# Optimization experiments

Hardware: AMD Instinct MI355X
Metric: run time of the kernel (lower is better)

Reference implementation:

```python
import jax, jax.numpy as jnp
import numpy as np

B = 262144
NODE_ROWS, EDGE_ROWS, D = 19, 36, 4
KEEP = 4


def _make_sparse(key, rows):
    # each sample has exactly KEEP nonzero rows at random (sorted) positions
    k1, k2 = jax.random.split(key)
    perm = jnp.argsort(jax.random.uniform(k1, (B, rows)), axis=1)
    idx = jnp.sort(perm[:, :KEEP], axis=1)                      # (B, KEEP)
    vals = jax.random.normal(k2, (B, KEEP, D), dtype=jnp.float32) + 0.1
    x = jnp.zeros((B, rows, D), dtype=jnp.float32)
    x = x.at[jnp.arange(B)[:, None], idx].set(vals)
    return x.reshape(B, rows * D)


def setup_inputs() -> dict:
    key = jax.random.key(0)
    kn, ke, k1, k2, k3 = jax.random.split(key, 5)
    node = _make_sparse(kn, NODE_ROWS)   # (B, 76)
    edge = _make_sparse(ke, EDGE_ROWS)   # (B, 144)
    # MLP params (torch Linear default-ish init, stored as (in, out))
    def lin(k, fin, fout):
        ka, kb = jax.random.split(k)
        s = 1.0 / np.sqrt(fin)
        W = jax.random.uniform(ka, (fin, fout), jnp.float32, -s, s)
        b = jax.random.uniform(kb, (fout,), jnp.float32, -s, s)
        return W, b
    W1, b1 = lin(k1, 32, 256)
    W2, b2 = lin(k2, 256, 128)
    W3, b3 = lin(k3, 128, 34)
    return {"node": node, "edge": edge, "W1": W1, "b1": b1,
            "W2": W2, "b2": b2, "W3": W3, "b3": b3}


def _compact4(x):
    # x: (B, R, D) -> first 4 nonzero rows per sample, order preserved: (B, 4, D)
    mask = jnp.any(x != 0, axis=-1)                              # (B, R)
    idx = jnp.argsort(~mask, axis=1, stable=True)[:, :KEEP]      # (B, 4)
    return jnp.take_along_axis(x, idx[:, :, None], axis=1)


def reference(node, edge, W1, b1, W2, b2, W3, b3):
    n = _compact4(node.reshape(-1, NODE_ROWS, D))                # (B, 4, 4)
    e = _compact4(edge.reshape(-1, EDGE_ROWS, D))                # (B, 4, 4)
    x = jnp.concatenate([n, e], axis=-2).reshape(-1, 8 * D)      # (B, 32)
    x = jax.nn.relu(x @ W1 + b1)
    x = jax.nn.relu(x @ W2 + b2)
    x = x @ W3 + b3                                              # (B, 34)
    return jax.nn.log_softmax(x, axis=1)
```

## Files before the change

kernel.cpp:

```cpp
#include <hip/hip_runtime.h>
#include <stdint.h>
#include <stddef.h>

typedef __bf16 bf16;
typedef __attribute__((ext_vector_type(8))) __bf16 bf16x8;
typedef __attribute__((ext_vector_type(4))) __bf16 bf16x4;
typedef __attribute__((ext_vector_type(4))) float  f32x4;
typedef __attribute__((ext_vector_type(16))) float f32x16;

#define W1OFF  0
#define W2OFF  (16*1024)
#define W3OFF  (80*1024)
#define BIOFF  (96*1024)
#define BI2OFF (BIOFF + 1024)
#define BI3OFF (BIOFF + 1536)
#define IMGSZ  (96*1024 + 1792)
#define NCHUNK (IMGSZ/16)
#define PERW   4096
#define LDSSZ  (IMGSZ + 8*PERW)

#define SWZ(s) ((((s)>>1)&3)<<4)

#define MFMA32(a,b,c) __builtin_amdgcn_mfma_f32_32x32x16_bf16((a),(b),(c),0,0,0)

__global__ void prep_kernel(const float* __restrict__ W1, const float* __restrict__ b1,
                            const float* __restrict__ W2, const float* __restrict__ b2,
                            const float* __restrict__ W3, const float* __restrict__ b3,
                            char* __restrict__ img)
{
  int tid = blockIdx.x * 256 + threadIdx.x;
  if (tid < 1024) {
    int frag = tid >> 6, l = tid & 63;
    int c = frag >> 1, t = frag & 1, hi = l >> 5;
    int n = c * 32 + (l & 31), k0 = t * 16 + 8 * hi;
    bf16x8 v;
    #pragma unroll
    for (int j = 0; j < 8; ++j) v[j] = (bf16)W1[(size_t)(k0 + j) * 256 + n];
    *(bf16x8*)(img + (size_t)tid * 16) = v;
  } else if (tid < 5120) {
    int e = tid - 1024, frag = e >> 6, l = e & 63;
    int nt2 = frag >> 4, c = (frag >> 1) & 7, t = frag & 1, hi = l >> 5;
    int n = nt2 * 32 + (l & 31), k0 = c * 32 + t * 16 + 8 * hi;
    bf16x8 v;
    #pragma unroll
    for (int j = 0; j < 8; ++j) v[j] = (bf16)W2[(size_t)(k0 + j) * 128 + n];
    *(bf16x8*)(img + W2OFF + (size_t)e * 16) = v;
  } else if (tid < 6144) {
    int e = tid - 5120, frag = e >> 6, l = e & 63;
    int nt3 = frag >> 3, c2 = (frag >> 1) & 3, t = frag & 1, hi = l >> 5;
    int n = nt3 * 32 + (l & 31), k0 = c2 * 32 + t * 16 + 8 * hi;
    bf16x8 v;
    #pragma unroll
    for (int j = 0; j < 8; ++j)
      v[j] = (n < 34) ? (bf16)W3[(size_t)(k0 + j) * 34 + n] : (bf16)0.f;
    *(bf16x8*)(img + W3OFF + (size_t)e * 16) = v;
  } else if (tid < 6144 + 448) {
    int e = tid - 6144;
    int le, chunk, idx; const float* bsrc; char* dst; int nb;
    if (e < 256)      { le = e;       bsrc = b1; dst = img + BIOFF;  nb = 34; chunk = le >> 5; }
    else if (e < 384) { le = e - 256; bsrc = b2; dst = img + BI2OFF; nb = 1000; chunk = le >> 5; }
    else              { le = e - 384; bsrc = b3; dst = img + BI3OFF; nb = 34; chunk = le >> 5; }
    idx = le & 31;
    int hi = idx >> 4, reg = idx & 15;
    int f = chunk * 32 + (reg & 3) + 8 * (reg >> 2) + 4 * hi;
    float v;
    if (e < 256)      v = b1[f];
    else if (e < 384) v = b2[f];
    else              v = (f < 34) ? b3[f] : 0.f;
    (void)bsrc; (void)nb;
    ((float*)dst)[le] = v;
  }
}

__global__ __launch_bounds__(512, 2) void mlp_kernel(
    const float* __restrict__ node, const float* __restrict__ edge,
    const char* __restrict__ img, float* __restrict__ out)
{
  __shared__ __align__(16) char sm[LDSSZ];
  const int tid  = threadIdx.x;
  const int lane = tid & 63;
  const int w    = tid >> 6;
  const int blk  = blockIdx.x;

  for (int c = tid; c < NCHUNK; c += 512)
    *(f32x4*)(sm + (size_t)c * 16) = *(const f32x4*)(img + (size_t)c * 16);
  __syncthreads();

  char* const xw  = sm + IMGSZ + w * PERW;
  char* const stg = xw + 2048;

  const int col = lane & 31;
  const int hi  = lane >> 5;
  const int swz = (col >> 1) & 3;
  const int cl  = lane & 3;
  const int sl  = lane >> 2;

  const float4* const np = (const float4*)node;
  const float4* const ep = (const float4*)edge;

  float4 nf[5], ef[9];

  auto issue_loads = [&](int sbase) {
    const int s = sbase + sl;
    #pragma unroll
    for (int i = 0; i < 5; ++i) {
      const int r = cl + 4 * i;
      nf[i] = (r < 19) ? np[(size_t)s * 19 + r] : make_float4(0.f, 0.f, 0.f, 0.f);
    }
    #pragma unroll
    for (int i = 0; i < 9; ++i)
      ef[i] = ep[(size_t)s * 36 + cl + 4 * i];
  };

  auto compact = [&](char* dst) {
    uint32_t nm = 0; unsigned long long em = 0;
    #pragma unroll
    for (int i = 0; i < 5; ++i) {
      const int r = cl + 4 * i;
      if (r < 19 && (nf[i].x != 0.f || nf[i].y != 0.f || nf[i].z != 0.f || nf[i].w != 0.f))
        nm |= (1u << r);
    }
    #pragma unroll
    for (int i = 0; i < 9; ++i) {
      const int r = cl + 4 * i;
      if (ef[i].x != 0.f || ef[i].y != 0.f || ef[i].z != 0.f || ef[i].w != 0.f)
        em |= (1ull << r);
    }
    nm |= __shfl_xor(nm, 1); nm |= __shfl_xor(nm, 2);
    em |= __shfl_xor(em, 1); em |= __shfl_xor(em, 2);
    bf16x4 zb; zb[0] = (bf16)0.f; zb[1] = (bf16)0.f; zb[2] = (bf16)0.f; zb[3] = (bf16)0.f;
    *(bf16x4*)(dst + sl * 64 + ((8 * cl)      ^ SWZ(sl))) = zb;
    *(bf16x4*)(dst + sl * 64 + ((8 * cl + 32) ^ SWZ(sl))) = zb;
    #pragma unroll
    for (int i = 0; i < 5; ++i) {
      const int r = cl + 4 * i;
      if (r < 19 && ((nm >> r) & 1u)) {
        const int slot = __popc(nm & ((1u << r) - 1u));
        if (slot < 4) {
          bf16x4 pk; pk[0] = (bf16)nf[i].x; pk[1] = (bf16)nf[i].y; pk[2] = (bf16)nf[i].z; pk[3] = (bf16)nf[i].w;
          *(bf16x4*)(dst + sl * 64 + ((8 * slot) ^ SWZ(sl))) = pk;
        }
      }
    }
    #pragma unroll
    for (int i = 0; i < 9; ++i) {
      const int r = cl + 4 * i;
      if ((em >> r) & 1ull) {
        const int slot = __popcll(em & ((1ull << r) - 1ull));
        if (slot < 4) {
          bf16x4 pk; pk[0] = (bf16)ef[i].x; pk[1] = (bf16)ef[i].y; pk[2] = (bf16)ef[i].z; pk[3] = (bf16)ef[i].w;
          *(bf16x4*)(dst + sl * 64 + ((32 + 8 * slot) ^ SWZ(sl))) = pk;
        }
      }
    }
  };

  auto ldbias = [&](const char* p) -> f32x16 {
    const f32x4* q4 = (const f32x4*)(p + hi * 64);
    f32x4 q0 = q4[0], q1 = q4[1], q2 = q4[2], q3 = q4[3];
    f32x16 r;
    #pragma unroll
    for (int i = 0; i < 4; ++i) { r[i] = q0[i]; r[4+i] = q1[i]; r[8+i] = q2[i]; r[12+i] = q3[i]; }
    return r;
  };

  #pragma unroll 1
  for (int p = 0; p < 4; ++p) {
    const int S = blk * 1024 + p * 256 + w * 32;

    issue_loads(S);       compact(xw);
    issue_loads(S + 16);  compact(xw + 1024);

    bf16x8 xf0 = *(const bf16x8*)(xw + col * 64 + ((hi * 16)      ^ SWZ(col)));
    bf16x8 xf1 = *(const bf16x8*)(xw + col * 64 + ((32 + hi * 16) ^ SWZ(col)));

    f32x16 acc2[4];
    #pragma unroll
    for (int nt2 = 0; nt2 < 4; ++nt2) acc2[nt2] = ldbias(sm + BI2OFF + nt2 * 128);

    #pragma unroll 1
    for (int c = 0; c < 8; ++c) {
      __builtin_amdgcn_sched_barrier(0);
      f32x16 d = ldbias(sm + BIOFF + c * 128);
      bf16x8 w10 = *(const bf16x8*)(sm + W1OFF + (c * 2 + 0) * 1024 + lane * 16);
      bf16x8 w11 = *(const bf16x8*)(sm + W1OFF + (c * 2 + 1) * 1024 + lane * 16);
      d = MFMA32(w10, xf0, d);
      d = MFMA32(w11, xf1, d);
      #pragma unroll
      for (int q = 0; q < 4; ++q) {
        bf16x4 pk;
        #pragma unroll
        for (int i = 0; i < 4; ++i) pk[i] = (bf16)fmaxf(d[4 * q + i], 0.f);
        *(bf16x4*)(stg + col * 64 + (((q ^ swz) << 4) + hi * 8)) = pk;
      }
      bf16x8 sf0 = *(const bf16x8*)(stg + col * 64 + (((0 + hi) ^ swz) << 4));
      bf16x8 sf1 = *(const bf16x8*)(stg + col * 64 + (((2 + hi) ^ swz) << 4));
      #pragma unroll
      for (int nt2 = 0; nt2 < 4; ++nt2) {
        bf16x8 a0 = *(const bf16x8*)(sm + W2OFF + ((nt2 * 8 + c) * 2 + 0) * 1024 + lane * 16);
        bf16x8 a1 = *(const bf16x8*)(sm + W2OFF + ((nt2 * 8 + c) * 2 + 1) * 1024 + lane * 16);
        acc2[nt2] = MFMA32(a0, sf0, acc2[nt2]);
        acc2[nt2] = MFMA32(a1, sf1, acc2[nt2]);
      }
    }

    f32x16 acc3[2];
    acc3[0] = ldbias(sm + BI3OFF + 0);
    acc3[1] = ldbias(sm + BI3OFF + 128);

    #pragma unroll
    for (int c2 = 0; c2 < 4; ++c2) {
      #pragma unroll
      for (int q = 0; q < 4; ++q) {
        bf16x4 pk;
        #pragma unroll
        for (int i = 0; i < 4; ++i) pk[i] = (bf16)fmaxf(acc2[c2][4 * q + i], 0.f);
        *(bf16x4*)(stg + col * 64 + (((q ^ swz) << 4) + hi * 8)) = pk;
      }
      bf16x8 sf0 = *(const bf16x8*)(stg + col * 64 + (((0 + hi) ^ swz) << 4));
      bf16x8 sf1 = *(const bf16x8*)(stg + col * 64 + (((2 + hi) ^ swz) << 4));
      #pragma unroll
      for (int nt3 = 0; nt3 < 2; ++nt3) {
        bf16x8 a0 = *(const bf16x8*)(sm + W3OFF + ((nt3 * 4 + c2) * 2 + 0) * 1024 + lane * 16);
        bf16x8 a1 = *(const bf16x8*)(sm + W3OFF + ((nt3 * 4 + c2) * 2 + 1) * 1024 + lane * 16);
        acc3[nt3] = MFMA32(a0, sf0, acc3[nt3]);
        acc3[nt3] = MFMA32(a1, sf1, acc3[nt3]);
      }
    }

    float mx = acc3[0][0];
    #pragma unroll
    for (int i = 1; i < 16; ++i) mx = fmaxf(mx, acc3[0][i]);
    if (hi == 0) { mx = fmaxf(mx, acc3[1][0]); mx = fmaxf(mx, acc3[1][1]); }
    mx = fmaxf(mx, __shfl_xor(mx, 32));
    float sum = 0.f;
    #pragma unroll
    for (int i = 0; i < 16; ++i) sum += __expf(acc3[0][i] - mx);
    if (hi == 0) sum += __expf(acc3[1][0] - mx) + __expf(acc3[1][1] - mx);
    sum += __shfl_xor(sum, 32);
    const float lse = mx + __logf(sum);

    float* orow = out + (size_t)(S + col) * 34;
    #pragma unroll
    for (int q = 0; q < 4; ++q) {
      *(float2*)(orow + 8 * q + 4 * hi)     = make_float2(acc3[0][4 * q]     - lse, acc3[0][4 * q + 1] - lse);
      *(float2*)(orow + 8 * q + 4 * hi + 2) = make_float2(acc3[0][4 * q + 2] - lse, acc3[0][4 * q + 3] - lse);
    }
    if (hi == 0)
      *(float2*)(orow + 32) = make_float2(acc3[1][0] - lse, acc3[1][1] - lse);
  }
}

extern "C" void kernel_launch(void* const* d_in, const int* in_sizes, int n_in,
                              void* d_out, int out_size, void* d_ws, size_t ws_size,
                              hipStream_t stream)
{
  const float* node = (const float*)d_in[0];
  const float* edge = (const float*)d_in[1];
  const float* W1   = (const float*)d_in[2];
  const float* b1   = (const float*)d_in[3];
  const float* W2   = (const float*)d_in[4];
  const float* b2   = (const float*)d_in[5];
  const float* W3   = (const float*)d_in[6];
  const float* b3   = (const float*)d_in[7];
  char* img = (char*)d_ws;

  prep_kernel<<<26, 256, 0, stream>>>(W1, b1, W2, b2, W3, b3, img);
  mlp_kernel<<<256, 512, 0, stream>>>(node, edge, img, (float*)d_out);
}
```

Measured before the change: 66.23 us.

## Process two 32-sample tiles per wave to reuse weight fragments across MFMAs

Each wave now handles 64 samples per iteration as two independent 32-sample tiles, A and B. Every W1/W2/W3 fragment read from LDS feeds two MFMAs instead of one, which halves LDS weight traffic per sample and gives the scheduler two independent MFMA chains to interleave. The cost is double the accumulator registers, so launch bounds drop to one block per CU and the per-wave LDS scratch grows to 6 KB. The lower occupancy may reduce latency hiding for the global input loads.

Measured after the change: 68.73 us. +3.8%, slower.

```diff
diff --git a/kernel.cpp b/kernel.cpp
--- a/kernel.cpp
+++ b/kernel.cpp
@@ -16,7 +16,7 @@
 #define BI3OFF (BIOFF + 1536)
 #define IMGSZ  (96*1024 + 1792)
 #define NCHUNK (IMGSZ/16)
-#define PERW   4096
+#define PERW   6144
 #define LDSSZ  (IMGSZ + 8*PERW)
 
 #define SWZ(s) ((((s)>>1)&3)<<4)
@@ -56,23 +56,24 @@
     *(bf16x8*)(img + W3OFF + (size_t)e * 16) = v;
   } else if (tid < 6144 + 448) {
     int e = tid - 6144;
-    int le, chunk, idx; const float* bsrc; char* dst; int nb;
-    if (e < 256)      { le = e;       bsrc = b1; dst = img + BIOFF;  nb = 34; chunk = le >> 5; }
-    else if (e < 384) { le = e - 256; bsrc = b2; dst = img + BI2OFF; nb = 1000; chunk = le >> 5; }
-    else              { le = e - 384; bsrc = b3; dst = img + BI3OFF; nb = 34; chunk = le >> 5; }
-    idx = le & 31;
+    int le, chunk;
+    char* dst;
+    if (e < 256)      { le = e;       dst = img + BIOFF;  }
+    else if (e < 384) { le = e - 256; dst = img + BI2OFF; }
+    else              { le = e - 384; dst = img + BI3OFF; }
+    chunk = le >> 5;
+    int idx = le & 31;
     int hi = idx >> 4, reg = idx & 15;
     int f = chunk * 32 + (reg & 3) + 8 * (reg >> 2) + 4 * hi;
     float v;
     if (e < 256)      v = b1[f];
     else if (e < 384) v = b2[f];
     else              v = (f < 34) ? b3[f] : 0.f;
-    (void)bsrc; (void)nb;
     ((float*)dst)[le] = v;
   }
 }
 
-__global__ __launch_bounds__(512, 2) void mlp_kernel(
+__global__ __launch_bounds__(512, 1) void mlp_kernel(
     const float* __restrict__ node, const float* __restrict__ edge,
     const char* __restrict__ img, float* __restrict__ out)
 {
@@ -87,7 +88,7 @@
   __syncthreads();
 
   char* const xw  = sm + IMGSZ + w * PERW;
-  char* const stg = xw + 2048;
+  char* const stg = xw + 4096;
 
   const int col = lane & 31;
   const int hi  = lane >> 5;
@@ -164,90 +165,118 @@
     return r;
   };
 
+  auto pack_stage = [&](const f32x16& d) {
+    #pragma unroll
+    for (int q = 0; q < 4; ++q) {
+      bf16x4 pk;
+      #pragma unroll
+      for (int i = 0; i < 4; ++i) pk[i] = (bf16)fmaxf(d[4 * q + i], 0.f);
+      *(bf16x4*)(stg + col * 64 + (((q ^ swz) << 4) + hi * 8)) = pk;
+    }
+  };
+
   #pragma unroll 1
-  for (int p = 0; p < 4; ++p) {
-    const int S = blk * 1024 + p * 256 + w * 32;
+  for (int p = 0; p < 2; ++p) {
+    const int S = blk * 1024 + p * 512 + w * 64;
 
     issue_loads(S);       compact(xw);
     issue_loads(S + 16);  compact(xw + 1024);
-
-    bf16x8 xf0 = *(const bf16x8*)(xw + col * 64 + ((hi * 16)      ^ SWZ(col)));
-    bf16x8 xf1 = *(const bf16x8*)(xw + col * 64 + ((32 + hi * 16) ^ SWZ(col)));
-
-    f32x16 acc2[4];
-    #pragma unroll
-    for (int nt2 = 0; nt2 < 4; ++nt2) acc2[nt2] = ldbias(sm + BI2OFF + nt2 * 128);
+    issue_loads(S + 32);  compact(xw + 2048);
+    issue_loads(S + 48);  compact(xw + 3072);
+
+    bf16x8 xfA0 = *(const bf16x8*)(xw        + col * 64 + ((hi * 16)      ^ SWZ(col)));
+    bf16x8 xfA1 = *(const bf16x8*)(xw        + col * 64 + ((32 + hi * 16) ^ SWZ(col)));
+    bf16x8 xfB0 = *(const bf16x8*)(xw + 2048 + col * 64 + ((hi * 16)      ^ SWZ(col)));
+    bf16x8 xfB1 = *(const bf16x8*)(xw + 2048 + col * 64 + ((32 + hi * 16) ^ SWZ(col)));
+
+    f32x16 acc2A[4], acc2B[4];
+    #pragma unroll
+    for (int nt2 = 0; nt2 < 4; ++nt2) {
+      f32x16 bi = ldbias(sm + BI2OFF + nt2 * 128);
+      acc2A[nt2] = bi; acc2B[nt2] = bi;
+    }
 
     #pragma unroll 1
     for (int c = 0; c < 8; ++c) {
       __builtin_amdgcn_sched_barrier(0);
-      f32x16 d = ldbias(sm + BIOFF + c * 128);
+      f32x16 dbias = ldbias(sm + BIOFF + c * 128);
       bf16x8 w10 = *(const bf16x8*)(sm + W1OFF + (c * 2 + 0) * 1024 + lane * 16);
       bf16x8 w11 = *(const bf16x8*)(sm + W1OFF + (c * 2 + 1) * 1024 + lane * 16);
-      d = MFMA32(w10, xf0, d);
-      d = MFMA32(w11, xf1, d);
-      #pragma unroll
-      for (int q = 0; q < 4; ++q) {
-        bf16x4 pk;
-        #pragma unroll
-        for (int i = 0; i < 4; ++i) pk[i] = (bf16)fmaxf(d[4 * q + i], 0.f);
-        *(bf16x4*)(stg + col * 64 + (((q ^ swz) << 4) + hi * 8)) = pk;
-      }
-      bf16x8 sf0 = *(const bf16x8*)(stg + col * 64 + (((0 + hi) ^ swz) << 4));
-      bf16x8 sf1 = *(const bf16x8*)(stg + col * 64 + (((2 + hi) ^ swz) << 4));
+      f32x16 dA = dbias, dB = dbias;
+      dA = MFMA32(w10, xfA0, dA);
+      dA = MFMA32(w11, xfA1, dA);
+      dB = MFMA32(w10, xfB0, dB);
+      dB = MFMA32(w11, xfB1, dB);
+
+      pack_stage(dA);
+      bf16x8 sfA0 = *(const bf16x8*)(stg + col * 64 + (((0 + hi) ^ swz) << 4));
+      bf16x8 sfA1 = *(const bf16x8*)(stg + col * 64 + (((2 + hi) ^ swz) << 4));
+      pack_stage(dB);
+      bf16x8 sfB0 = *(const bf16x8*)(stg + col * 64 + (((0 + hi) ^ swz) << 4));
+      bf16x8 sfB1 = *(const bf16x8*)(stg + col * 64 + (((2 + hi) ^ swz) << 4));
+
       #pragma unroll
       for (int nt2 = 0; nt2 < 4; ++nt2) {
         bf16x8 a0 = *(const bf16x8*)(sm + W2OFF + ((nt2 * 8 + c) * 2 + 0) * 1024 + lane * 16);
         bf16x8 a1 = *(const bf16x8*)(sm + W2OFF + ((nt2 * 8 + c) * 2 + 1) * 1024 + lane * 16);
-        acc2[nt2] = MFMA32(a0, sf0, acc2[nt2]);
-        acc2[nt2] = MFMA32(a1, sf1, acc2[nt2]);
-      }
-    }
-
-    f32x16 acc3[2];
-    acc3[0] = ldbias(sm + BI3OFF + 0);
-    acc3[1] = ldbias(sm + BI3OFF + 128);
+        acc2A[nt2] = MFMA32(a0, sfA0, acc2A[nt2]);
+        acc2A[nt2] = MFMA32(a1, sfA1, acc2A[nt2]);
+        acc2B[nt2] = MFMA32(a0, sfB0, acc2B[nt2]);
+        acc2B[nt2] = MFMA32(a1, sfB1, acc2B[nt2]);
+      }
+    }
+
+    f32x16 acc3A[2], acc3B[2];
+    {
+      f32x16 b30 = ldbias(sm + BI3OFF + 0);
+      f32x16 b31 = ldbias(sm + BI3OFF + 128);
+      acc3A[0] = b30; acc3B[0] = b30;
+      acc3A[1] = b31; acc3B[1] = b31;
+    }
 
     #pragma unroll
     for (int c2 = 0; c2 < 4; ++c2) {
-      #pragma unroll
-      for (int q = 0; q < 4; ++q) {
-        bf16x4 pk;
-        #pragma unroll
-        for (int i = 0; i < 4; ++i) pk[i] = (bf16)fmaxf(acc2[c2][4 * q + i], 0.f);
-        *(bf16x4*)(stg + col * 64 + (((q ^ swz) << 4) + hi * 8)) = pk;
-      }
-      bf16x8 sf0 = *(const bf16x8*)(stg + col * 64 + (((0 + hi) ^ swz) << 4));
-      bf16x8 sf1 = *(const bf16x8*)(stg + col * 64 + (((2 + hi) ^ swz) << 4));
+      pack_stage(acc2A[c2]);
+      bf16x8 sfA0 = *(const bf16x8*)(stg + col * 64 + (((0 + hi) ^ swz) << 4));
+      bf16x8 sfA1 = *(const bf16x8*)(stg + col * 64 + (((2 + hi) ^ swz) << 4));
+      pack_stage(acc2B[c2]);
+      bf16x8 sfB0 = *(const bf16x8*)(stg + col * 64 + (((0 + hi) ^ swz) << 4));
+      bf16x8 sfB1 = *(const bf16x8*)(stg + col * 64 + (((2 + hi) ^ swz) << 4));
       #pragma unroll
       for (int nt3 = 0; nt3 < 2; ++nt3) {
         bf16x8 a0 = *(const bf16x8*)(sm + W3OFF + ((nt3 * 4 + c2) * 2 + 0) * 1024 + lane * 16);
         bf16x8 a1 = *(const bf16x8*)(sm + W3OFF + ((nt3 * 4 + c2) * 2 + 1) * 1024 + lane * 16);
-        acc3[nt3] = MFMA32(a0, sf0, acc3[nt3]);
-        acc3[nt3] = MFMA32(a1, sf1, acc3[nt3]);
-      }
-    }
-
-    float mx = acc3[0][0];
-    #pragma unroll
-    for (int i = 1; i < 16; ++i) mx = fmaxf(mx, acc3[0][i]);
-    if (hi == 0) { mx = fmaxf(mx, acc3[1][0]); mx = fmaxf(mx, acc3[1][1]); }
-    mx = fmaxf(mx, __shfl_xor(mx, 32));
-    float sum = 0.f;
-    #pragma unroll
-    for (int i = 0; i < 16; ++i) sum += __expf(acc3[0][i] - mx);
-    if (hi == 0) sum += __expf(acc3[1][0] - mx) + __expf(acc3[1][1] - mx);
-    sum += __shfl_xor(sum, 32);
-    const float lse = mx + __logf(sum);
-
-    float* orow = out + (size_t)(S + col) * 34;
-    #pragma unroll
-    for (int q = 0; q < 4; ++q) {
-      *(float2*)(orow + 8 * q + 4 * hi)     = make_float2(acc3[0][4 * q]     - lse, acc3[0][4 * q + 1] - lse);
-      *(float2*)(orow + 8 * q + 4 * hi + 2) = make_float2(acc3[0][4 * q + 2] - lse, acc3[0][4 * q + 3] - lse);
-    }
-    if (hi == 0)
-      *(float2*)(orow + 32) = make_float2(acc3[1][0] - lse, acc3[1][1] - lse);
+        acc3A[nt3] = MFMA32(a0, sfA0, acc3A[nt3]);
+        acc3A[nt3] = MFMA32(a1, sfA1, acc3A[nt3]);
+        acc3B[nt3] = MFMA32(a0, sfB0, acc3B[nt3]);
+        acc3B[nt3] = MFMA32(a1, sfB1, acc3B[nt3]);
+      }
+    }
+
+    #pragma unroll
+    for (int tb = 0; tb < 2; ++tb) {
+      const f32x16* a3 = tb ? acc3B : acc3A;
+      float mx = a3[0][0];
+      #pragma unroll
+      for (int i = 1; i < 16; ++i) mx = fmaxf(mx, a3[0][i]);
+      if (hi == 0) { mx = fmaxf(mx, a3[1][0]); mx = fmaxf(mx, a3[1][1]); }
+      mx = fmaxf(mx, __shfl_xor(mx, 32));
+      float sum = 0.f;
+      #pragma unroll
+      for (int i = 0; i < 16; ++i) sum += __expf(a3[0][i] - mx);
+      if (hi == 0) sum += __expf(a3[1][0] - mx) + __expf(a3[1][1] - mx);
+      sum += __shfl_xor(sum, 32);
+      const float lse = mx + __logf(sum);
+
+      float* orow = out + (size_t)(S + tb * 32 + col) * 34;
+      #pragma unroll
+      for (int q = 0; q < 4; ++q) {
+        *(float2*)(orow + 8 * q + 4 * hi)     = make_float2(a3[0][4 * q]     - lse, a3[0][4 * q + 1] - lse);
+        *(float2*)(orow + 8 * q + 4 * hi + 2) = make_float2(a3[0][4 * q + 2] - lse, a3[0][4 * q + 3] - lse);
+      }
+      if (hi == 0)
+        *(float2*)(orow + 32) = make_float2(a3[1][0] - lse, a3[1][1] - lse);
+    }
   }
 }
 
```
